# Kernel optimization log

Measured on AMD Instinct MI355X. Metric: run time of the kernel, lower is better.

## Reference

```python
import jax, jax.numpy as jnp
import numpy as np

T = 5       # fixed temporal factor in the original forward
HEADS = 8
DIM = 512
DIM_HEAD = 64
INNER = HEADS * DIM_HEAD  # 512 (must equal DIM for the masked scatter)


def setup_inputs() -> dict:
    key = jax.random.key(0)
    ks = jax.random.split(key, 8)
    bt, n = 40, 3137  # b=8, t=5; n-1 = 56*56 visual tokens
    x = jax.random.normal(ks[0], (bt, n, DIM), dtype=jnp.float32)
    mask = jax.random.randint(ks[1], (bt, 56, 56), 0, 2).astype(jnp.float32)
    s = 1.0 / np.sqrt(DIM)
    w_vq = jax.random.normal(ks[2], (DIM, INNER), dtype=jnp.float32) * s
    w_vkv = jax.random.normal(ks[3], (DIM, 2 * INNER), dtype=jnp.float32) * s
    w_aqkv = jax.random.normal(ks[4], (DIM, 3 * INNER), dtype=jnp.float32) * s
    w_out = jax.random.normal(ks[5], (INNER, DIM), dtype=jnp.float32) * s
    b_out = jnp.zeros((DIM,), dtype=jnp.float32)
    return {"x": x, "mask": mask, "w_vq": w_vq, "w_vkv": w_vkv,
            "w_aqkv": w_aqkv, "w_out": w_out, "b_out": b_out}


def reference(x, mask, w_vq, w_vkv, w_aqkv, w_out, b_out):
    bt, n, dim = x.shape
    b = bt // T
    nv = n - 1
    dh = DIM_HEAD
    scale = dh ** -0.5

    A = x[:, 0]        # (bt, dim) -- single 'action' token per frame
    V = x[:, 1:]       # (bt, nv, dim)
    m = mask.reshape(bt, nv, 1)

    aq, ak, av = jnp.split(A @ w_aqkv, 3, axis=-1)      # each (bt, INNER)
    vk, vv = jnp.split(V @ w_vkv, 2, axis=-1)           # each (bt, nv, INNER)
    vq = V @ w_vq                                        # (bt, nv, INNER)

    # --- A -> V cross attention: per batch, T A-queries over T*nv V keys ---
    qa = aq.reshape(b, T, HEADS, dh)
    Kv = vk.reshape(b, T * nv, HEADS, dh)
    Vv = vv.reshape(b, T * nv, HEADS, dh)
    av_dots = jnp.einsum('bqhd,bkhd->bhqk', qa, Kv) * scale
    av_attn = jax.nn.softmax(av_dots, axis=-1)
    av_o = jnp.einsum('bhqk,bkhd->bqhd', av_attn, Vv)   # (b, T, H, dh)
    a_out = av_o.reshape(bt, 1, INNER)

    # --- V -> A cross attention with block mask: every V token attends only
    # to its own batch's T A-tokens (the -inf block fill in the original) ---
    Qv = vq.reshape(b, T, nv, HEADS, dh)
    Ka = ak.reshape(b, T, HEADS, dh)
    Va = av.reshape(b, T, HEADS, dh)
    va_dots = jnp.einsum('bfnhd,bkhd->bhfnk', Qv, Ka) * scale
    va_attn = jax.nn.softmax(va_dots, axis=-1)          # softmax over T keys
    va_o = jnp.einsum('bhfnk,bkhd->bfnhd', va_attn, Va)
    v_full = va_o.reshape(bt, nv, INNER)

    # original: scatter attn out into V.clone() then * mask, under no_grad()
    # => masked positions get attention output, others V*0 = 0; detached.
    v_out = jax.lax.stop_gradient(v_full * m)

    out = jnp.concatenate([a_out, v_out], axis=1)       # (bt, n, INNER)
    return out @ w_out + b_out
```

## Files before the change

### kernel.cpp

```cpp
#include <hip/hip_runtime.h>

typedef unsigned short u16;
typedef unsigned int u32;
typedef __attribute__((ext_vector_type(8))) u16 u16x8;
typedef __attribute__((ext_vector_type(8))) __bf16 bf16x8;
typedef __attribute__((ext_vector_type(4))) float f32x4;

__device__ __forceinline__ float b2f(u16 u){ return __uint_as_float(((u32)u)<<16); }
__device__ __forceinline__ u16 f2b(float f){
  u32 b = __float_as_uint(f);
  return (u16)((b + 0x7fffu + ((b>>16)&1u))>>16);
}
__device__ __forceinline__ void gload16(const void* g, void* l){
  __builtin_amdgcn_global_load_lds((__attribute__((address_space(1))) void*)g,
                                   (__attribute__((address_space(3))) void*)l, 16, 0, 0);
}
__device__ __forceinline__ float wred_max(float v){
#pragma unroll
  for (int o=32;o>0;o>>=1) v = fmaxf(v, __shfl_xor(v,o));
  return v;
}
__device__ __forceinline__ float wred_sum(float v){
#pragma unroll
  for (int o=32;o>0;o>>=1) v += __shfl_xor(v,o);
  return v;
}


__global__ void k_pre(const float* __restrict__ x, const float* __restrict__ wvq,
                      const float* __restrict__ wvkv, const float* __restrict__ wout,
                      const float* __restrict__ waqkv,
                      u16* __restrict__ xb, u16* __restrict__ W1T,
                      u16* __restrict__ WoutT, float* __restrict__ aqkv){
  const int bid = blockIdx.x, tid = threadIdx.x;
  if (bid < 2048){
    const int stride = 2048*256;
    for (int i = bid*256 + tid; i < 8030720; i += stride){
      const float4* p = (const float4*)(x + (size_t)i*8);
      float4 a = p[0], b = p[1];
      u16x8 o;
      o[0]=f2b(a.x); o[1]=f2b(a.y); o[2]=f2b(a.z); o[3]=f2b(a.w);
      o[4]=f2b(b.x); o[5]=f2b(b.y); o[6]=f2b(b.z); o[7]=f2b(b.w);
      *(u16x8*)(xb + (size_t)i*8) = o;
    }
  } else if (bid < 6144){
    int id = (bid-2048)*256 + tid;
    if (id < 786432){
      int n = id >> 9, k = id & 511;
      float v;
      if (n < 512){
        v = wvq[k*512 + n];
      } else {
        int j = n - 512, h = j >> 7, r = j & 127;
        int c2 = (r < 64) ? (h*64 + r) : (512 + h*64 + (r - 64));
        v = wvkv[k*1024 + c2];
      }
      W1T[id] = f2b(v);
    } else {
      int j = id - 786432;
      int n = j >> 9, k = j & 511;
      WoutT[j] = f2b(wout[k*512 + n]);
    }
  } else {
    int id = (bid-6144)*256 + tid;
    int bt = id / 1536, c = id % 1536;
    const float* xr = x + (size_t)bt*3137*512;
    float s = 0.f;
    for (int k=0;k<512;k++) s += xr[k]*waqkv[k*1536+c];
    aqkv[id] = s;
  }
}

template<int FOUT>
__global__ __launch_bounds__(512, 2) void k_gemm8p(
    const u16* __restrict__ A, const u16* __restrict__ BT,
    int M, int N, int K, int NX,
    u16* __restrict__ Cb, float* __restrict__ Cf, const float* __restrict__ bias)
{
  __shared__ __align__(16) char Ls[131072];
  char* LA = Ls;
  char* LB = Ls + 65536;
  const int tid = threadIdx.x;
  const int wid = tid >> 6, lane = tid & 63;
  const int wm = wid >> 2, wn = wid & 3;
  const int nwg = gridDim.x, orig = blockIdx.x;
  const int q8 = nwg >> 3, r8 = nwg & 7;
  const int xc = orig & 7, sl = orig >> 3;
  const int work = (xc < r8 ? xc*(q8+1) : r8*(q8+1) + (xc-r8)*q8) + sl;
  const int m0 = (work / NX) * 256, n0 = (work % NX) * 256;
  const size_t K2 = (size_t)K * 2;
  const char* Ab = (const char*)A;
  const char* Bb = (const char*)BT;
  size_t asrch[2], bsrch[2];
#pragma unroll
  for (int h=0; h<2; h++){
    int ra = m0 + h*128 + wid*16 + (lane & 15);
    if (ra >= M) ra = M - 1;
    asrch[h] = (size_t)ra * K2 + ((lane >> 4) << 4);
    bsrch[h] = (size_t)(n0 + h*128 + wid*16 + (lane & 15)) * K2 + ((lane >> 4) << 4);
  }
  const int sd0 = wid*2048;

#define STG_A(d,h,kt) { size_t ko = (size_t)(kt)*128; \
    gload16(Ab + asrch[h] + ko,      LA + (d)*32768 + (h)*16384 + sd0); \
    gload16(Ab + asrch[h] + ko + 64, LA + (d)*32768 + (h)*16384 + sd0 + 1024); }
#define STG_B(d,h,kt) { size_t ko = (size_t)(kt)*128; \
    gload16(Bb + bsrch[h] + ko,      LB + (d)*32768 + (h)*16384 + sd0); \
    gload16(Bb + bsrch[h] + ko + 64, LB + (d)*32768 + (h)*16384 + sd0 + 1024); }

  bf16x8 afr[4][2], bfr[2][2];
#define RD_A(d,QM) { const char* ab_ = LA + (d)*32768 + (QM)*16384 + wm*8192 + lane*16; \
    _Pragma("unroll") for (int fm=0; fm<4; fm++){ \
      afr[fm][0] = *(const bf16x8*)(ab_ + fm*2048); \
      afr[fm][1] = *(const bf16x8*)(ab_ + fm*2048 + 1024); } }
#define RD_B(d,QN) { const char* bb_ = LB + (d)*32768 + (QN)*16384 + wn*4096 + lane*16; \
    _Pragma("unroll") for (int fn=0; fn<2; fn++){ \
      bfr[fn][0] = *(const bf16x8*)(bb_ + fn*2048); \
      bfr[fn][1] = *(const bf16x8*)(bb_ + fn*2048 + 1024); } }

  f32x4 acc[8][4] = {};
#define MFMA16(QM,QN) { \
    _Pragma("unroll") for (int fm=0; fm<4; fm++){ \
      _Pragma("unroll") for (int fn=0; fn<2; fn++){ \
        acc[(QM)*4+fm][(QN)*2+fn] = __builtin_amdgcn_mfma_f32_16x16x32_bf16( \
            afr[fm][0], bfr[fn][0], acc[(QM)*4+fm][(QN)*2+fn], 0,0,0); \
        acc[(QM)*4+fm][(QN)*2+fn] = __builtin_amdgcn_mfma_f32_16x16x32_bf16( \
            afr[fm][1], bfr[fn][1], acc[(QM)*4+fm][(QN)*2+fn], 0,0,0); } } }

#define PH_MID(QM,QN) \
    __builtin_amdgcn_sched_barrier(0); \
    __builtin_amdgcn_s_barrier(); \
    asm volatile("s_waitcnt lgkmcnt(0)" ::: "memory"); \
    __builtin_amdgcn_sched_barrier(0); \
    __builtin_amdgcn_s_setprio(1); \
    MFMA16(QM,QN) \
    __builtin_amdgcn_s_setprio(0); \
    __builtin_amdgcn_sched_barrier(0);
#define BAR __builtin_amdgcn_s_barrier()

  const int NI = K >> 7;
  STG_A(0,0,0) STG_B(0,1,0) STG_A(0,1,0) STG_B(0,0,0) STG_A(1,0,1) STG_B(1,1,1)
  asm volatile("s_waitcnt vmcnt(4)" ::: "memory");
  BAR;

  for (int it = 0; it < NI; ++it){
    const int t1 = 2*it + 1, t2 = 2*it + 2, t3 = 2*it + 3;
    const bool more = (it + 1 < NI);
    RD_A(0,0) RD_B(0,0) STG_A(1,1,t1)
    PH_MID(0,0) BAR;
    RD_B(0,1) STG_B(1,0,t1)
    PH_MID(0,1) BAR;
    RD_A(0,1) if (more){ STG_A(0,0,t2) }
    PH_MID(1,1) BAR;
    RD_B(0,0) if (more){ STG_B(0,1,t2) }
    PH_MID(1,0)
    if (more) { asm volatile("s_waitcnt vmcnt(4)" ::: "memory"); }
    else      { asm volatile("s_waitcnt vmcnt(0)" ::: "memory"); }
    BAR;
    RD_A(1,0) RD_B(1,0) if (more){ STG_A(0,1,t2) }
    PH_MID(0,0) BAR;
    RD_B(1,1) if (more){ STG_B(0,0,t2) }
    PH_MID(0,1) BAR;
    RD_A(1,1) if (more){ STG_A(1,0,t3) }
    PH_MID(1,1) BAR;
    RD_B(1,0) if (more){ STG_B(1,1,t3) }
    PH_MID(1,0)
    if (more) { asm volatile("s_waitcnt vmcnt(4)" ::: "memory"); }
    BAR;
  }
#undef STG_A
#undef STG_B
#undef RD_A
#undef RD_B
#undef MFMA16
#undef PH_MID
#undef BAR
  if (m0 + 256 <= M){
#pragma unroll
    for (int mi=0; mi<8; mi++){
      const int rb = m0 + (mi>>2)*128 + wm*64 + (mi&3)*16 + ((lane>>4)<<2);
#pragma unroll
      for (int ni=0; ni<4; ni++){
        const int col = n0 + (ni>>1)*128 + wn*32 + (ni&1)*16 + (lane&15);
#pragma unroll
        for (int rg=0; rg<4; rg++){
          float v = acc[mi][ni][rg];
          if (FOUT) Cf[(size_t)(rb+rg)*N + col] = v + bias[col];
          else      Cb[(size_t)(rb+rg)*N + col] = f2b(v);
        }
      }
    }
  } else {
#pragma unroll
    for (int mi=0; mi<8; mi++){
      const int rb = m0 + (mi>>2)*128 + wm*64 + (mi&3)*16 + ((lane>>4)<<2);
#pragma unroll
      for (int ni=0; ni<4; ni++){
        const int col = n0 + (ni>>1)*128 + wn*32 + (ni&1)*16 + (lane&15);
#pragma unroll
        for (int rg=0; rg<4; rg++){
          if (rb + rg < M){
            float v = acc[mi][ni][rg];
            if (FOUT) Cf[(size_t)(rb+rg)*N + col] = v + bias[col];
            else      Cb[(size_t)(rb+rg)*N + col] = f2b(v);
          }
        }
      }
    }
  }
}

__global__ __launch_bounds__(320) void k_attn_agent(
    const u16* __restrict__ out1, const float* __restrict__ aqkv,
    float* __restrict__ pm, float* __restrict__ pl, float* __restrict__ pacc)
{
  __shared__ __align__(16) char Ksm[16384];
  __shared__ __align__(16) char Vsm[16384];
  const int bid = blockIdx.x;
  const int sp = bid & 15, bh = bid >> 4, b = bh >> 3, h = bh & 7;
  const int tid = threadIdx.x, wid = tid >> 6, lane = tid & 63;
  const int q = wid;
  float qreg[64];
  {
    const float* ap = aqkv + ((size_t)(b*5+q)*1536 + h*64);
#pragma unroll
    for (int d=0; d<64; d++) qreg[d] = ap[d];
  }
  float m = -1e30f, l = 0.f;
  float acc[8] = {0,0,0,0,0,0,0,0};
  const int g0 = sp * 980;
  for (int c = 0; c < 8; c++){
    for (int idx = tid; idx < 2048; idx += 320){
      int r = idx >> 4, g = idx & 15;
      int loc = c*128 + r; if (loc > 979) loc = 979;
      int gk = g0 + loc;
      int tk = gk / 3136, nv = gk - tk*3136;
      size_t grow = (size_t)((b*5+tk)*3137 + 1 + nv)*1536 + 512 + h*128 + g*8;
      u16x8 v = *(const u16x8*)(out1 + grow);
      char* dst = (g < 8) ? Ksm : Vsm;
      int seg = g & 7;
      *(u16x8*)(dst + r*128 + ((seg*16) ^ ((r&7)<<4))) = v;
    }
    __syncthreads();
    float s0 = 0.f, s1 = 0.f;
#pragma unroll
    for (int seg=0; seg<8; seg++){
      const int r0 = lane, r1 = 64 + lane;
      u16x8 k0 = *(const u16x8*)(Ksm + r0*128 + ((seg*16) ^ ((r0&7)<<4)));
      u16x8 k1 = *(const u16x8*)(Ksm + r1*128 + ((seg*16) ^ ((r1&7)<<4)));
#pragma unroll
      for (int j=0;j<8;j++){
        s0 += qreg[seg*8+j]*b2f(k0[j]);
        s1 += qreg[seg*8+j]*b2f(k1[j]);
      }
    }
    s0 *= 0.125f; s1 *= 0.125f;
    const int locbase = c*128;
    if (locbase + lane >= 980)      s0 = -1e30f;
    if (locbase + 64 + lane >= 980) s1 = -1e30f;
    float cmax = wred_max(fmaxf(s0, s1));
    float mn = fmaxf(m, cmax);
    float resc = __expf(m - mn);
    float p0 = (s0 > -1e29f) ? __expf(s0 - mn) : 0.f;
    float p1 = (s1 > -1e29f) ? __expf(s1 - mn) : 0.f;
    l = l*resc + wred_sum(p0 + p1);
#pragma unroll
    for (int j=0;j<8;j++) acc[j] *= resc;
    const int g = lane >> 3, cc = lane & 7;
#pragma unroll
    for (int i=0;i<16;i++){
      int k = i*8 + g;
      u16x8 vv = *(const u16x8*)(Vsm + k*128 + ((cc*16) ^ ((k&7)<<4)));
      float p = (i < 8) ? __shfl(p0, k) : __shfl(p1, k-64);
#pragma unroll
      for (int j=0;j<8;j++) acc[j] += p*b2f(vv[j]);
    }
    m = mn;
    __syncthreads();
  }
#pragma unroll
  for (int j=0;j<8;j++){
    float v = acc[j];
    v += __shfl_xor(v, 8); v += __shfl_xor(v, 16); v += __shfl_xor(v, 32);
    acc[j] = v;
  }
  const int base = (bh*16 + sp)*5 + q;
  if (lane == 0){ pm[base] = m; pl[base] = l; }
  if (lane < 8){
    float* pa = pacc + (size_t)base*64 + lane*8;
#pragma unroll
    for (int j=0;j<8;j++) pa[j] = acc[j];
  }
}

__global__ __launch_bounds__(256) void k_attn_frame(
    const u16* __restrict__ out1, const float* __restrict__ aqkv,
    const float* __restrict__ mask, const float* __restrict__ pm,
    const float* __restrict__ pl, const float* __restrict__ pacc,
    u16* __restrict__ IN)
{
  const int bid = blockIdx.x, tid = threadIdx.x;
  if (bid < 3920){
    __shared__ float Ka[5][8][68];
    __shared__ float Va[5][8][68];
    const int b = bid / 490, bx = bid % 490;
    for (int i = tid; i < 2560; i += 256){
      int t = i >> 9, rem = i & 511, hh = rem >> 6, d = rem & 63;
      const float* src = aqkv + (size_t)(b*5+t)*1536;
      Ka[t][hh][d] = src[512 + hh*64 + d];
      Va[t][hh][d] = src[1024 + hh*64 + d];
    }
    __syncthreads();
    const int task = bx*256 + tid;
    const int h = task & 7, rl = task >> 3;
    const int f = rl / 3136, nv = rl - f*3136;
    const int bt = b*5 + f;
    const size_t r1 = (size_t)bt*3137 + 1 + nv;
    const u16* qp = out1 + r1*1536 + h*64;
    float qf[64];
#pragma unroll
    for (int sg=0; sg<8; sg++){
      u16x8 v = *(const u16x8*)(qp + sg*8);
#pragma unroll
      for (int j=0;j<8;j++) qf[sg*8+j] = b2f(v[j]);
    }
    float sd[5];
#pragma unroll
    for (int t=0;t<5;t++){
      float s = 0.f;
#pragma unroll
      for (int d=0;d<64;d++) s += qf[d]*Ka[t][h][d];
      sd[t] = s*0.125f;
    }
    float mx = sd[0];
#pragma unroll
    for (int t=1;t<5;t++) mx = fmaxf(mx, sd[t]);
    float p[5], ps = 0.f;
#pragma unroll
    for (int t=0;t<5;t++){ p[t] = __expf(sd[t]-mx); ps += p[t]; }
    const float mv = mask[(size_t)bt*3136 + nv] / ps;
    u16* op = IN + r1*512 + h*64;
#pragma unroll
    for (int sg=0; sg<8; sg++){
      u16x8 o;
#pragma unroll
      for (int j=0;j<8;j++){
        const int d = sg*8+j;
        float v = 0.f;
#pragma unroll
        for (int t=0;t<5;t++) v += p[t]*Va[t][h][d];
        o[j] = f2b(v*mv);
      }
      *(u16x8*)(op + sg*8) = o;
    }
  } else {
    const int id = (bid - 3920)*4 + (tid >> 6);
    const int d = tid & 63;
    const int q = id % 5, t2 = id / 5;
    const int h = t2 & 7, b = t2 >> 3;
    const int bh = b*8 + h;
    float ms = -1e30f;
#pragma unroll
    for (int s2=0;s2<16;s2++) ms = fmaxf(ms, pm[(bh*16+s2)*5+q]);
    float L = 0.f, o = 0.f;
#pragma unroll
    for (int s2=0;s2<16;s2++){
      int base = (bh*16+s2)*5+q;
      float w = __expf(pm[base]-ms);
      L += w*pl[base];
      o += w*pacc[(size_t)base*64 + d];
    }
    IN[(size_t)(b*5+q)*3137*512 + h*64 + d] = f2b(o / L);
  }
}

extern "C" void kernel_launch(void* const* d_in, const int* in_sizes, int n_in,
                              void* d_out, int out_size, void* d_ws, size_t ws_size,
                              hipStream_t stream)
{
  const float* x      = (const float*)d_in[0];
  const float* mask   = (const float*)d_in[1];
  const float* w_vq   = (const float*)d_in[2];
  const float* w_vkv  = (const float*)d_in[3];
  const float* w_aqkv = (const float*)d_in[4];
  const float* w_out  = (const float*)d_in[5];
  const float* b_out  = (const float*)d_in[6];
  float* out = (float*)d_out;
  char* ws = (char*)d_ws;

  constexpr size_t MR = 125480;
  constexpr size_t OFF_XB   = 0;
  constexpr size_t OFF_OUT1 = OFF_XB + MR*512*2;
  constexpr size_t OFF_W1T  = OFF_OUT1 + MR*1536*2;
  constexpr size_t OFF_WOT  = OFF_W1T + 1536*512*2;
  constexpr size_t OFF_AQKV = OFF_WOT + 512*512*2;
  constexpr size_t OFF_PM   = OFF_AQKV + 40*1536*4;
  constexpr size_t OFF_PL   = OFF_PM + 5120*4;
  constexpr size_t OFF_PACC = OFF_PL + 5120*4;

  u16* Xb     = (u16*)(ws + OFF_XB);
  u16* out1   = (u16*)(ws + OFF_OUT1);
  u16* W1T    = (u16*)(ws + OFF_W1T);
  u16* WoutT  = (u16*)(ws + OFF_WOT);
  float* aqkv = (float*)(ws + OFF_AQKV);
  float* pm   = (float*)(ws + OFF_PM);
  float* pl   = (float*)(ws + OFF_PL);
  float* pacc = (float*)(ws + OFF_PACC);

  k_pre<<<6384, 256, 0, stream>>>(x, w_vq, w_vkv, w_out, w_aqkv, Xb, W1T, WoutT, aqkv);
  k_gemm8p<0><<<2946, 512, 0, stream>>>(Xb, W1T, (int)MR, 1536, 512, 6,
                                        out1, nullptr, nullptr);
  k_attn_agent<<<1024, 320, 0, stream>>>(out1, aqkv, pm, pl, pacc);
  k_attn_frame<<<4000, 256, 0, stream>>>(out1, aqkv, mask, pm, pl, pacc, Xb);
  k_gemm8p<1><<<982, 512, 0, stream>>>(Xb, WoutT, (int)MR, 512, 512, 2,
                                       nullptr, out, b_out);
}
```

Measured before the change: 774.6 us.

## Compact masked rows and skip zero-mask work in Q projection and output GEMM

Builds a compacted list of rows whose mask is nonzero (plus the action-token rows) with a ballot and atomic in the prep kernel. The Q projection and the output projection become gathered GEMMs over those rows only. Masked-out visual rows get the bias written directly by a new fill kernel, and the frame-attention kernel skips them. This removes about half of the Q-projection and output-GEMM FLOPs for a mask that is about half zeros, at the cost of indirect row addressing, an extra split GEMM launch and some grid blocks that exit early.

```diff
diff --git a/kernel.cpp b/kernel.cpp
--- a/kernel.cpp
+++ b/kernel.cpp
@@ -27,11 +27,30 @@
 }
 
 
+__global__ void k_biasfill(const float* __restrict__ mask, const float* __restrict__ b_out,
+                           float* __restrict__ out, u32* __restrict__ cnt){
+  if (blockIdx.x == 0 && threadIdx.x == 0) *cnt = 0u;
+  const int lane = threadIdx.x & 63;
+  const int gw = (blockIdx.x*256 + threadIdx.x) >> 6;
+  const int nw = (gridDim.x*256) >> 6;
+  float4 bv0 = *(const float4*)(b_out + lane*8);
+  float4 bv1 = *(const float4*)(b_out + lane*8 + 4);
+  for (int r = gw; r < 125440; r += nw){
+    if (mask[r] == 0.f){
+      int bt = r / 3136, nv = r - bt*3136;
+      float* op = out + ((size_t)bt*3137 + 1 + nv)*512 + lane*8;
+      *(float4*)op = bv0;
+      *(float4*)(op+4) = bv1;
+    }
+  }
+}
+
 __global__ void k_pre(const float* __restrict__ x, const float* __restrict__ wvq,
                       const float* __restrict__ wvkv, const float* __restrict__ wout,
-                      const float* __restrict__ waqkv,
+                      const float* __restrict__ waqkv, const float* __restrict__ mask,
                       u16* __restrict__ xb, u16* __restrict__ W1T,
-                      u16* __restrict__ WoutT, float* __restrict__ aqkv){
+                      u16* __restrict__ WoutT, float* __restrict__ aqkv,
+                      u32* __restrict__ rowlist, u32* __restrict__ cnt){
   const int bid = blockIdx.x, tid = threadIdx.x;
   if (bid < 2048){
     const int stride = 2048*256;
@@ -61,21 +80,42 @@
       int n = j >> 9, k = j & 511;
       WoutT[j] = f2b(wout[k*512 + n]);
     }
-  } else {
+  } else if (bid < 6384){
     int id = (bid-6144)*256 + tid;
     int bt = id / 1536, c = id % 1536;
     const float* xr = x + (size_t)bt*3137*512;
     float s = 0.f;
     for (int k=0;k<512;k++) s += xr[k]*waqkv[k*1536+c];
     aqkv[id] = s;
-  }
-}
-
-template<int FOUT>
+  } else {
+    int j = (bid-6384)*256 + tid;
+    bool pred = false; u32 row = 0;
+    if (j < 125440){
+      int bt = j / 3136, nv = j - bt*3136;
+      pred = (mask[j] != 0.f);
+      row = (u32)(bt*3137 + 1 + nv);
+    } else if (j < 125480){
+      pred = true;
+      row = (u32)((j - 125440) * 3137);
+    }
+    unsigned long long bal = __ballot(pred);
+    const int lane = tid & 63;
+    u32 base = 0;
+    if (lane == 0 && bal) base = atomicAdd(cnt, (u32)__popcll(bal));
+    base = __shfl(base, 0);
+    if (pred){
+      int pos = __popcll(bal & ((1ull << lane) - 1ull));
+      rowlist[base + pos] = row;
+    }
+  }
+}
+
+template<int MODE>
 __global__ __launch_bounds__(512, 2) void k_gemm8p(
     const u16* __restrict__ A, const u16* __restrict__ BT,
-    int M, int N, int K, int NX,
-    u16* __restrict__ Cb, float* __restrict__ Cf, const float* __restrict__ bias)
+    int M, int N, int K, int NX, int ldc, int coff,
+    u16* __restrict__ Cb, float* __restrict__ Cf, const float* __restrict__ bias,
+    const u32* __restrict__ rowlist, const u32* __restrict__ cntp)
 {
   __shared__ __align__(16) char Ls[131072];
   char* LA = Ls;
@@ -83,11 +123,14 @@
   const int tid = threadIdx.x;
   const int wid = tid >> 6, lane = tid & 63;
   const int wm = wid >> 2, wn = wid & 3;
+  int Mg = M;
+  if (MODE != 0) Mg = (int)*cntp;
   const int nwg = gridDim.x, orig = blockIdx.x;
   const int q8 = nwg >> 3, r8 = nwg & 7;
   const int xc = orig & 7, sl = orig >> 3;
   const int work = (xc < r8 ? xc*(q8+1) : r8*(q8+1) + (xc-r8)*q8) + sl;
   const int m0 = (work / NX) * 256, n0 = (work % NX) * 256;
+  if (MODE != 0 && m0 >= Mg) return;
   const size_t K2 = (size_t)K * 2;
   const char* Ab = (const char*)A;
   const char* Bb = (const char*)BT;
@@ -95,8 +138,9 @@
 #pragma unroll
   for (int h=0; h<2; h++){
     int ra = m0 + h*128 + wid*16 + (lane & 15);
-    if (ra >= M) ra = M - 1;
-    asrch[h] = (size_t)ra * K2 + ((lane >> 4) << 4);
+    if (ra >= Mg) ra = Mg - 1;
+    size_t arow = (MODE == 0) ? (size_t)ra : (size_t)rowlist[ra];
+    asrch[h] = arow * K2 + ((lane >> 4) << 4);
     bsrch[h] = (size_t)(n0 + h*128 + wid*16 + (lane & 15)) * K2 + ((lane >> 4) << 4);
   }
   const int sd0 = wid*2048;
@@ -175,18 +219,21 @@
 #undef MFMA16
 #undef PH_MID
 #undef BAR
-  if (m0 + 256 <= M){
+  const bool full = (m0 + 256 <= Mg);
+  if (full){
 #pragma unroll
     for (int mi=0; mi<8; mi++){
       const int rb = m0 + (mi>>2)*128 + wm*64 + (mi&3)*16 + ((lane>>4)<<2);
 #pragma unroll
-      for (int ni=0; ni<4; ni++){
-        const int col = n0 + (ni>>1)*128 + wn*32 + (ni&1)*16 + (lane&15);
-#pragma unroll
-        for (int rg=0; rg<4; rg++){
+      for (int rg=0; rg<4; rg++){
+        const int r = rb + rg;
+        const size_t orow = (MODE == 0) ? (size_t)r : (size_t)rowlist[r];
+#pragma unroll
+        for (int ni=0; ni<4; ni++){
+          const int col = n0 + (ni>>1)*128 + wn*32 + (ni&1)*16 + (lane&15);
           float v = acc[mi][ni][rg];
-          if (FOUT) Cf[(size_t)(rb+rg)*N + col] = v + bias[col];
-          else      Cb[(size_t)(rb+rg)*N + col] = f2b(v);
+          if (MODE == 2) Cf[orow*(size_t)ldc + col] = v + bias[col];
+          else           Cb[orow*(size_t)ldc + coff + col] = f2b(v);
         }
       }
     }
@@ -195,14 +242,16 @@
     for (int mi=0; mi<8; mi++){
       const int rb = m0 + (mi>>2)*128 + wm*64 + (mi&3)*16 + ((lane>>4)<<2);
 #pragma unroll
-      for (int ni=0; ni<4; ni++){
-        const int col = n0 + (ni>>1)*128 + wn*32 + (ni&1)*16 + (lane&15);
-#pragma unroll
-        for (int rg=0; rg<4; rg++){
-          if (rb + rg < M){
+      for (int rg=0; rg<4; rg++){
+        const int r = rb + rg;
+        if (r < Mg){
+          const size_t orow = (MODE == 0) ? (size_t)r : (size_t)rowlist[r];
+#pragma unroll
+          for (int ni=0; ni<4; ni++){
+            const int col = n0 + (ni>>1)*128 + wn*32 + (ni&1)*16 + (lane&15);
             float v = acc[mi][ni][rg];
-            if (FOUT) Cf[(size_t)(rb+rg)*N + col] = v + bias[col];
-            else      Cb[(size_t)(rb+rg)*N + col] = f2b(v);
+            if (MODE == 2) Cf[orow*(size_t)ldc + col] = v + bias[col];
+            else           Cb[orow*(size_t)ldc + coff + col] = f2b(v);
           }
         }
       }
@@ -316,42 +365,45 @@
     const int f = rl / 3136, nv = rl - f*3136;
     const int bt = b*5 + f;
     const size_t r1 = (size_t)bt*3137 + 1 + nv;
-    const u16* qp = out1 + r1*1536 + h*64;
-    float qf[64];
-#pragma unroll
-    for (int sg=0; sg<8; sg++){
-      u16x8 v = *(const u16x8*)(qp + sg*8);
-#pragma unroll
-      for (int j=0;j<8;j++) qf[sg*8+j] = b2f(v[j]);
-    }
-    float sd[5];
-#pragma unroll
-    for (int t=0;t<5;t++){
-      float s = 0.f;
-#pragma unroll
-      for (int d=0;d<64;d++) s += qf[d]*Ka[t][h][d];
-      sd[t] = s*0.125f;
-    }
-    float mx = sd[0];
-#pragma unroll
-    for (int t=1;t<5;t++) mx = fmaxf(mx, sd[t]);
-    float p[5], ps = 0.f;
-#pragma unroll
-    for (int t=0;t<5;t++){ p[t] = __expf(sd[t]-mx); ps += p[t]; }
-    const float mv = mask[(size_t)bt*3136 + nv] / ps;
-    u16* op = IN + r1*512 + h*64;
-#pragma unroll
-    for (int sg=0; sg<8; sg++){
-      u16x8 o;
-#pragma unroll
-      for (int j=0;j<8;j++){
-        const int d = sg*8+j;
-        float v = 0.f;
-#pragma unroll
-        for (int t=0;t<5;t++) v += p[t]*Va[t][h][d];
-        o[j] = f2b(v*mv);
-      }
-      *(u16x8*)(op + sg*8) = o;
+    const float mraw = mask[(size_t)bt*3136 + nv];
+    if (mraw != 0.f){
+      const u16* qp = out1 + r1*1536 + h*64;
+      float qf[64];
+#pragma unroll
+      for (int sg=0; sg<8; sg++){
+        u16x8 v = *(const u16x8*)(qp + sg*8);
+#pragma unroll
+        for (int j=0;j<8;j++) qf[sg*8+j] = b2f(v[j]);
+      }
+      float sd[5];
+#pragma unroll
+      for (int t=0;t<5;t++){
+        float s = 0.f;
+#pragma unroll
+        for (int d=0;d<64;d++) s += qf[d]*Ka[t][h][d];
+        sd[t] = s*0.125f;
+      }
+      float mx = sd[0];
+#pragma unroll
+      for (int t=1;t<5;t++) mx = fmaxf(mx, sd[t]);
+      float p[5], ps = 0.f;
+#pragma unroll
+      for (int t=0;t<5;t++){ p[t] = __expf(sd[t]-mx); ps += p[t]; }
+      const float mv = mraw / ps;
+      u16* op = IN + r1*512 + h*64;
+#pragma unroll
+      for (int sg=0; sg<8; sg++){
+        u16x8 o;
+#pragma unroll
+        for (int j=0;j<8;j++){
+          const int d = sg*8+j;
+          float v = 0.f;
+#pragma unroll
+          for (int t=0;t<5;t++) v += p[t]*Va[t][h][d];
+          o[j] = f2b(v*mv);
+        }
+        *(u16x8*)(op + sg*8) = o;
+      }
     }
   } else {
     const int id = (bid - 3920)*4 + (tid >> 6);
@@ -397,6 +449,8 @@
   constexpr size_t OFF_PM   = OFF_AQKV + 40*1536*4;
   constexpr size_t OFF_PL   = OFF_PM + 5120*4;
   constexpr size_t OFF_PACC = OFF_PL + 5120*4;
+  constexpr size_t OFF_ROWS = OFF_PACC + 5120*64*4;
+  constexpr size_t OFF_CNT  = OFF_ROWS + MR*4;
 
   u16* Xb     = (u16*)(ws + OFF_XB);
   u16* out1   = (u16*)(ws + OFF_OUT1);
@@ -406,12 +460,21 @@
   float* pm   = (float*)(ws + OFF_PM);
   float* pl   = (float*)(ws + OFF_PL);
   float* pacc = (float*)(ws + OFF_PACC);
-
-  k_pre<<<6384, 256, 0, stream>>>(x, w_vq, w_vkv, w_out, w_aqkv, Xb, W1T, WoutT, aqkv);
-  k_gemm8p<0><<<2946, 512, 0, stream>>>(Xb, W1T, (int)MR, 1536, 512, 6,
-                                        out1, nullptr, nullptr);
+  u32* rows   = (u32*)(ws + OFF_ROWS);
+  u32* cnt    = (u32*)(ws + OFF_CNT);
+
+  k_biasfill<<<2048, 256, 0, stream>>>(mask, b_out, out, cnt);
+  k_pre<<<6875, 256, 0, stream>>>(x, w_vq, w_vkv, w_out, w_aqkv, mask,
+                                  Xb, W1T, WoutT, aqkv, rows, cnt);
+  k_gemm8p<0><<<1964, 512, 0, stream>>>(Xb, W1T + 512*512, (int)MR, 1024, 512, 4,
+                                        1536, 512, out1, nullptr, nullptr,
+                                        nullptr, nullptr);
+  k_gemm8p<1><<<982, 512, 0, stream>>>(Xb, W1T, (int)MR, 512, 512, 2,
+                                       1536, 0, out1, nullptr, nullptr,
+                                       rows, cnt);
   k_attn_agent<<<1024, 320, 0, stream>>>(out1, aqkv, pm, pl, pacc);
   k_attn_frame<<<4000, 256, 0, stream>>>(out1, aqkv, mask, pm, pl, pacc, Xb);
-  k_gemm8p<1><<<982, 512, 0, stream>>>(Xb, WoutT, (int)MR, 512, 512, 2,
-                                       nullptr, out, b_out);
-}
+  k_gemm8p<2><<<982, 512, 0, stream>>>(Xb, WoutT, (int)MR, 512, 512, 2,
+                                       512, 0, nullptr, out, b_out,
+                                       rows, cnt);
+}
```

After: 798.0 us. 3.0% more time.
